# Performance work log

Measured on AMD Instinct MI355X. Metric: run time of the kernel, lower is better.

Reference implementation:

```python
import jax, jax.numpy as jnp
import numpy as np
import itertools

DIM = 384; KEY_DIM = 32; NH = 8; RES = 7; N = RES * RES
D = 4 * KEY_DIM; DH = D * NH; NHKD = KEY_DIM * NH; HID = 4 * DIM
B = 512
SCALE = KEY_DIM ** -0.5

def ste_round(x):
    return x + jax.lax.stop_gradient(jnp.round(x) - x)

def ste_floor(x):
    return x + jax.lax.stop_gradient(jnp.floor(x) - x)

def quant_act(x, bits=8):
    # dynamic per-tensor symmetric fake-quant (QuantAct)
    qmax = 2.0 ** (bits - 1) - 1
    s = jnp.maximum(jnp.max(jnp.abs(x)) / qmax, 1e-8)
    return jnp.clip(ste_round(x / s), -qmax, qmax) * s, s

def quant_w(w, bits=8):
    # per-output-channel symmetric weight fake-quant
    qmax = 2.0 ** (bits - 1) - 1
    red = tuple(range(1, w.ndim))
    s = jnp.maximum(jnp.max(jnp.abs(w), axis=red, keepdims=True) / qmax, 1e-8)
    return jnp.clip(ste_round(w / s), -qmax, qmax) * s

def conv(x, w, b, stride=1, pad=0, groups=1):
    # QuantBNConv2d with BN folded into (w, b)
    y = jax.lax.conv_general_dilated(
        x, quant_w(w), (stride, stride), [(pad, pad), (pad, pad)],
        dimension_numbers=('NCHW', 'OIHW', 'NCHW'), feature_group_count=groups)
    return y + b[None, :, None, None]

def head_mix(attn, w, b):
    # talking-heads 1x1 QuantConv2d over the head axis
    return jnp.einsum('oi,bixy->boxy', quant_w(w)[:, :, 0, 0], attn) + b[None, :, None, None]

def int_softmax(x, sf, out_bit=16):
    # I-BERT style integer softmax (2nd-order poly approx of exp) over last axis
    n = 30
    c0 = 0.35815147
    x_int = x / sf
    x_int = x_int - jnp.max(x_int, axis=-1, keepdims=True)
    x0_int = jnp.floor(-0.6931 / sf)  # ln(2) in integer domain
    x_int = jnp.maximum(x_int, n * x0_int)
    q = ste_floor(x_int / x0_int)
    r = x_int - x0_int * q
    b_int = jnp.floor((0.96963238 / c0) / sf)
    c_int = jnp.floor((1.0 / c0) / (sf * sf))
    z = (r + b_int) * r + c_int
    exp_int = jnp.clip(ste_floor(z * jnp.exp2(n - q)), 0.0, None)
    exp, exp_sf = quant_act(exp_int * (c0 * sf * sf / 2.0 ** n), 16)
    exp_int = exp / exp_sf
    factor = ste_floor(2.0 ** 32 / jnp.sum(exp_int, axis=-1, keepdims=True))
    exp_int = ste_floor(exp_int * factor / 2.0 ** (32 - out_bit))
    sf_out = 1.0 / 2.0 ** out_bit
    return exp_int * sf_out, sf_out

def _forward(x, act_sf, wq, bq, wk, bk, wv, bv, wvl, bvl, attn_biases,
             wth1, bth1, wth2, bth2, wproj, bproj,
             wfc1, bfc1, wmid, bmid, wfc2, bfc2, ls1, ls2, bias_idxs):
    Bn = x.shape[0]
    # --- token mixer (Q_Attention4D, stride=None) ---
    q, _ = quant_act(conv(x, wq, bq))
    q = q.reshape(Bn, NH, KEY_DIM, N).transpose(0, 1, 3, 2)   # (B,H,N,kd)
    k, _ = quant_act(conv(x, wk, bk))
    k = k.reshape(Bn, NH, KEY_DIM, N)                          # (B,H,kd,N)
    vf, _ = quant_act(conv(x, wv, bv))
    vl, _ = quant_act(conv(vf, wvl, bvl, pad=1, groups=DH))    # depthwise 3x3 local branch
    v = vf.reshape(Bn, NH, D, N).transpose(0, 1, 3, 2)         # (B,H,N,d)
    attn = jnp.einsum('bhnk,bhkm->bhnm', q, k) * SCALE
    attn = attn + attn_biases[:, bias_idxs]                    # (H,N,N) relative position bias
    attn, _ = quant_act(attn, 8)                               # quant_pre_th1
    attn = head_mix(attn, wth1, bth1)                          # talking_head1
    attn, a_sf = quant_act(attn, 8)                            # quant_attn
    attn, a_sf = int_softmax(attn, a_sf, 16)
    attn = head_mix(attn, wth2, bth2)                          # talking_head2
    attn, _ = quant_act(attn, 8)                               # quant_postsm
    out = jnp.einsum('bhnm,bhmd->bhnd', attn, v)
    out = out.transpose(0, 1, 3, 2).reshape(Bn, DH, RES, RES) + vl
    out, _ = quant_act(out)                                    # quant_av_res
    out = jax.nn.relu(out)                                     # proj_act
    out, _ = quant_act(out)                                    # proj_in_quant
    out = conv(out, wproj, bproj)
    out, _ = quant_act(out)                                    # proj_quant
    x1, _ = quant_act(x + ls1[None] * out)                     # residual 1 + quant_res1
    # --- Q_Mlp (mid_conv=True, ReLU) ---
    h = jax.nn.relu(conv(x1, wfc1, bfc1))
    h, _ = quant_act(h)
    h = jax.nn.relu(conv(h, wmid, bmid, pad=1, groups=HID))
    h, _ = quant_act(h)
    h = conv(h, wfc2, bfc2)
    h, _ = quant_act(h)
    out2, out_sf = quant_act(x1 + ls2[None] * h)               # residual 2 + quant_res2
    return out2, out_sf

def setup_inputs():
    key = jax.random.key(0)
    ks = jax.random.split(key, 16)
    rn = lambda k, shp: (0.02 * jax.random.normal(k, shp)).astype(jnp.float32)
    z = lambda n: jnp.zeros((n,), jnp.float32)
    # rebuild attention_bias_idxs exactly as in __init__
    pts = list(itertools.product(range(RES), range(RES)))
    offs, idxs = {}, []
    for p1 in pts:
        for p2 in pts:
            o = (abs(p1[0] - p2[0]), abs(p1[1] - p2[1]))
            if o not in offs:
                offs[o] = len(offs)
            idxs.append(offs[o])
    bias_idxs = jnp.asarray(np.array(idxs, dtype=np.int32).reshape(N, N))
    return dict(
        x=jax.random.normal(ks[0], (B, DIM, RES, RES), jnp.float32),
        act_sf=jnp.ones((1,), jnp.float32),
        wq=rn(ks[1], (NHKD, DIM, 1, 1)), bq=z(NHKD),
        wk=rn(ks[2], (NHKD, DIM, 1, 1)), bk=z(NHKD),
        wv=rn(ks[3], (DH, DIM, 1, 1)), bv=z(DH),
        wvl=rn(ks[4], (DH, 1, 3, 3)), bvl=z(DH),
        attn_biases=rn(ks[5], (NH, len(offs))),
        wth1=rn(ks[6], (NH, NH, 1, 1)), bth1=z(NH),
        wth2=rn(ks[7], (NH, NH, 1, 1)), bth2=z(NH),
        wproj=rn(ks[8], (DIM, DH, 1, 1)), bproj=z(DIM),
        wfc1=rn(ks[9], (HID, DIM, 1, 1)), bfc1=z(HID),
        wmid=rn(ks[10], (HID, 1, 3, 3)), bmid=z(HID),
        wfc2=rn(ks[11], (DIM, HID, 1, 1)), bfc2=z(DIM),
        ls1=1e-5 * jnp.ones((DIM, 1, 1), jnp.float32),
        ls2=1e-5 * jnp.ones((DIM, 1, 1), jnp.float32),
        bias_idxs=bias_idxs)

def reference(x, act_sf, wq, bq, wk, bk, wv, bv, wvl, bvl, attn_biases,
              wth1, bth1, wth2, bth2, wproj, bproj,
              wfc1, bfc1, wmid, bmid, wfc2, bfc2, ls1, ls2, bias_idxs):
    return _forward(x, act_sf, wq, bq, wk, bk, wv, bv, wvl, bvl, attn_biases,
                    wth1, bth1, wth2, bth2, wproj, bproj,
                    wfc1, bfc1, wmid, bmid, wfc2, bfc2, ls1, ls2, bias_idxs)
```

## Files before the change

kernel.cpp:

```cpp
#include <hip/hip_runtime.h>

typedef unsigned short u16;
typedef unsigned int u32;
typedef float f32x4 __attribute__((ext_vector_type(4)));
typedef short bf16x8 __attribute__((ext_vector_type(8)));
typedef short s16x4 __attribute__((ext_vector_type(4)));


__device__ __forceinline__ u16 f2bf(float f){
  u32 x = __float_as_uint(f);
  x += 0x7fffu + ((x >> 16) & 1u);
  return (u16)(x >> 16);
}
__device__ __forceinline__ float bf2f(u16 u){ return __uint_as_float(((u32)u) << 16); }
__device__ __forceinline__ float qsc(float m, float qmax){ return fmaxf(m / qmax, 1e-8f); }
__device__ __forceinline__ float fq(float x, float s){
  return fminf(fmaxf(rintf(x / s), -127.f), 127.f) * s;
}
__device__ __forceinline__ float fqi(float x, float s, float inv){
  return fminf(fmaxf(rintf(x * inv), -127.f), 127.f) * s;
}
__device__ __forceinline__ float rdmx(const float* mx, int reg){
  float m = mx[reg];
  #pragma unroll
  for (int s = 1; s < 16; ++s) m = fmaxf(m, mx[s*64 + reg]);
  return m;
}
__device__ __forceinline__ void blockMaxTo(float* mx, int reg, float v){
  __shared__ float red[8];
  #pragma unroll
  for (int o = 32; o > 0; o >>= 1) v = fmaxf(v, __shfl_xor(v, o, 64));
  const int wid = threadIdx.x >> 6;
  const int nw = (int)(blockDim.x + 63) >> 6;
  __syncthreads();
  if ((threadIdx.x & 63) == 0) red[wid] = v;
  __syncthreads();
  if (threadIdx.x == 0){
    float m = red[0];
    for (int i = 1; i < nw; ++i) m = fmaxf(m, red[i]);
    const int slot = (blockIdx.x + blockIdx.y*4) & 15;
    atomicMax((int*)&mx[slot*64 + reg], __float_as_int(m));
  }
}
__device__ __forceinline__ void blockMax2To(float* mx, int r0i, float v0, int r1i, float v1){
  __shared__ float r0[8], r1[8];
  #pragma unroll
  for (int o = 32; o > 0; o >>= 1){
    v0 = fmaxf(v0, __shfl_xor(v0, o, 64));
    v1 = fmaxf(v1, __shfl_xor(v1, o, 64));
  }
  const int wid = threadIdx.x >> 6;
  const int nw = (int)(blockDim.x + 63) >> 6;
  __syncthreads();
  if ((threadIdx.x & 63) == 0){ r0[wid] = v0; r1[wid] = v1; }
  __syncthreads();
  if (threadIdx.x == 0){
    float m0 = r0[0], m1 = r1[0];
    for (int i = 1; i < nw; ++i){ m0 = fmaxf(m0, r0[i]); m1 = fmaxf(m1, r1[i]); }
    const int slot = (blockIdx.x + blockIdx.y*4) & 15;
    atomicMax((int*)&mx[slot*64 + r0i], __float_as_int(m0));
    atomicMax((int*)&mx[slot*64 + r1i], __float_as_int(m1));
  }
}

__device__ __forceinline__ void gload16(const void* g, void* l){
  __builtin_amdgcn_global_load_lds((const __attribute__((address_space(1))) u32*)g,
                                   (__attribute__((address_space(3))) u32*)l, 16, 0, 0);
}

__global__ void zeromx(float* mx){
  for (int j = threadIdx.x; j < 1024; j += 256) mx[j] = 0.f;
}

__global__ __launch_bounds__(128) void wquant(
    const float* wq, const float* wk, const float* wv, const float* wproj,
    const float* wfc1, const float* wfc2, const float* wvl, const float* wmid,
    const float* wth1, const float* wth2,
    const float* bq, const float* bk, const float* bv,
    const float* ab, const int* idxs,
    u16* wqkv_b, u16* wproj_b, u16* wfc1_b, u16* wfc2_b,
    float* wvl_q, float* wmid_q, float* wth1_q, float* wth2_q, float* biasqkv,
    float* biasx)
{
  const int tid = threadIdx.x;
  const int bid = blockIdx.x;
  if (bid == 6416){
    for (int j = tid; j < 1536; j += 128){
      float v = (j < 256) ? bq[j] : ((j < 512) ? bk[j - 256] : bv[j - 512]);
      biasqkv[j] = v;
    }
    return;
  }
  if (bid >= 6417){
    const int h = bid - 6417;
    for (int j = tid; j < 2401; j += 128)
      biasx[h*2401 + j] = ab[h*49 + idxs[j]];
    return;
  }
  const int rows[10] = {256,256,1024,384,1536,384,1024,1536,8,8};
  int seg = 0, r = bid;
  while (r >= rows[seg]) { r -= rows[seg]; ++seg; }
  int len = 0;
  const float* src = nullptr; u16* db = nullptr; float* df = nullptr;
  switch (seg){
    case 0: len = 384;  src = wq    + r*384;  db = wqkv_b + r*384;        break;
    case 1: len = 384;  src = wk    + r*384;  db = wqkv_b + (256+r)*384;  break;
    case 2: len = 384;  src = wv    + r*384;  db = wqkv_b + (512+r)*384;  break;
    case 3: len = 1024; src = wproj + r*1024; db = wproj_b + r*1024;      break;
    case 4: len = 384;  src = wfc1  + r*384;  db = wfc1_b + r*384;        break;
    case 5: len = 1536; src = wfc2  + r*1536; db = wfc2_b + r*1536;       break;
    case 6: len = 9;    src = wvl   + r*9;    df = wvl_q + r*9;           break;
    case 7: len = 9;    src = wmid  + r*9;    df = wmid_q + r*9;          break;
    case 8: len = 8;    src = wth1  + r*8;    df = wth1_q + r*8;          break;
    default: len = 8;   src = wth2  + r*8;    df = wth2_q + r*8;          break;
  }
  float lm = 0.f;
  for (int j = tid; j < len; j += 128) lm = fmaxf(lm, fabsf(src[j]));
  __shared__ float red[128];
  red[tid] = lm; __syncthreads();
  for (int s = 64; s > 0; s >>= 1){
    if (tid < s) red[tid] = fmaxf(red[tid], red[tid + s]);
    __syncthreads();
  }
  float s = fmaxf(red[0] / 127.f, 1e-8f);
  for (int j = tid; j < len; j += 128){
    float v = fminf(fmaxf(rintf(src[j] / s), -127.f), 127.f) * s;
    if (db) db[j] = f2bf(v); else df[j] = v;
  }
}

__global__ __launch_bounds__(256) void xpose(const float* __restrict__ x, u16* __restrict__ xT){
  const int b = blockIdx.x;
  __shared__ u16 xb[18816];
  const int tid = threadIdx.x;
  for (int jj = tid; jj < 4704; jj += 256){
    const float4 v = *(const float4*)&x[(size_t)b*18816 + jj*4];
    xb[jj*4+0] = f2bf(v.x); xb[jj*4+1] = f2bf(v.y);
    xb[jj*4+2] = f2bf(v.z); xb[jj*4+3] = f2bf(v.w);
  }
  __syncthreads();
  for (int jj = tid; jj < 4704; jj += 256){
    int j = jj*4, p = j / 384, c = j - p*384;
    s16x4 o;
    #pragma unroll
    for (int u = 0; u < 4; ++u) o[u] = (short)xb[(c+u)*49 + p];
    *(s16x4*)&xT[(size_t)b*18816 + j] = o;
  }
}

__global__ __launch_bounds__(256, 3) void gemm_bt(
    const u16* __restrict__ A, const u16* __restrict__ Bt,
    const float* __restrict__ bias, u16* __restrict__ C,
    float* __restrict__ mx, int N, int K, int epi, int region, int aquant)
{
  const int nx = gridDim.x;
  const int nwg = nx * gridDim.y;
  const int orig = blockIdx.x + nx * blockIdx.y;
  const int q8 = nwg >> 3, r8 = nwg & 7;
  const int xcd = orig & 7;
  const int lid = ((xcd < r8) ? xcd*(q8+1) : r8*(q8+1) + (xcd - r8)*q8) + (orig >> 3);
  const int n0 = (lid % nx) * 128;
  const int m0 = (lid / nx) * 128;
  __shared__ __align__(16) u16 As[128*64];
  __shared__ __align__(16) u16 Bs[128*64];
  const int tid = threadIdx.x;
  const int lane = tid & 63, wid = tid >> 6;
  const int wr = wid >> 1, wc = wid & 1;
  float qa_s0 = 1.f, qa_i0 = 1.f, qa_s1 = 1.f, qa_i1 = 1.f;
  if (aquant == 1){
    qa_s0 = qsc(rdmx(mx,7), 127.f); qa_i0 = 1.f/qa_s0;
    float posq = fq(rdmx(mx,8), qa_s0);
    qa_s1 = fmaxf(posq / 127.f, 1e-8f); qa_i1 = 1.f/qa_s1;
  } else if (aquant == 2){
    qa_s0 = qsc(rdmx(mx,12), 127.f); qa_i0 = 1.f/qa_s0;
  }
  f32x4 acc[4][4] = {};
  const int nsteps = K >> 6;
  for (int s = 0; s < nsteps; ++s){
    const int k0 = s << 6;
    #pragma unroll
    for (int j = 0; j < 4; ++j){
      int boff = j*4096 + tid*16;
      int row = boff >> 7;
      int ce  = (((boff & 127) ^ ((row & 7) << 4)) >> 1);
      if (aquant == 0){
        gload16(A + (size_t)(m0 + row)*K + k0 + ce, (char*)As + boff);
      } else {
        uint4 va = *(const uint4*)(A + (size_t)(m0 + row)*K + k0 + ce);
        u16* e = (u16*)&va;
        #pragma unroll
        for (int u = 0; u < 8; ++u){
          float f = bf2f(e[u]);
          if (aquant == 1){
            f = fmaxf(fqi(f, qa_s0, qa_i0), 0.f);
            f = fqi(f, qa_s1, qa_i1);
          } else {
            f = fqi(f, qa_s0, qa_i0);
          }
          e[u] = f2bf(f);
        }
        *(uint4*)((char*)As + boff) = va;
      }
      gload16(Bt + (size_t)(n0 + row)*K + k0 + ce, (char*)Bs + boff);
    }
    __syncthreads();
    #pragma unroll
    for (int kk = 0; kk < 2; ++kk){
      bf16x8 af[4], bfr[4];
      #pragma unroll
      for (int i = 0; i < 4; ++i){
        int ar = wr*64 + i*16 + (lane & 15);
        int aidx = (ar*64 + kk*32 + (lane >> 4)*8) ^ ((ar & 7) << 3);
        af[i]  = *(const bf16x8*)&As[aidx];
        int br = wc*64 + i*16 + (lane & 15);
        int bidx = (br*64 + kk*32 + (lane >> 4)*8) ^ ((br & 7) << 3);
        bfr[i] = *(const bf16x8*)&Bs[bidx];
      }
      #pragma unroll
      for (int i = 0; i < 4; ++i){
        #pragma unroll
        for (int j = 0; j < 4; ++j){
          acc[i][j] = __builtin_amdgcn_mfma_f32_16x16x32_bf16(af[i], bfr[j], acc[i][j], 0, 0, 0);
        }
      }
    }
    __syncthreads();
  }
  float lm = 0.f;
  #pragma unroll
  for (int i = 0; i < 4; ++i){
    int rbase = m0 + wr*64 + i*16 + ((lane >> 4) << 2);
    #pragma unroll
    for (int j = 0; j < 4; ++j){
      int col = n0 + wc*64 + j*16 + (lane & 15);
      float bv = bias[col];
      #pragma unroll
      for (int q = 0; q < 4; ++q){
        float v = acc[i][j][q] + bv;
        if (epi == 2) v = fmaxf(v, 0.f);
        C[(size_t)(rbase + q)*N + col] = f2bf(v);
        lm = fmaxf(lm, (epi == 2) ? v : fabsf(v));
      }
    }
  }
  int reg = region;
  if (epi == 1) reg = (n0 < 256) ? 0 : ((n0 < 512) ? 1 : 2);
  blockMaxTo(mx, reg, lm);
}

__global__ __launch_bounds__(256) void attn_qk(
    const u16* __restrict__ qkv, const float* __restrict__ biasx,
    const float* __restrict__ wv9, const float* __restrict__ bvl,
    u16* __restrict__ S, u16* __restrict__ vlb, float* __restrict__ mx)
{
  const int h = blockIdx.x;
  __shared__ __align__(16) float xin[6272];
  __shared__ __align__(16) u16 Qb[64*40];
  __shared__ __align__(16) u16 Kb[64*40];
  const float sq = qsc(rdmx(mx,0), 127.f), sk = qsc(rdmx(mx,1), 127.f), sv = qsc(rdmx(mx,2), 127.f);
  const float iq = 1.f/sq, ik = 1.f/sk, iv = 1.f/sv;
  const int tid = threadIdx.x;
  const int lane = tid & 63, wid = tid >> 6;
  const int c = tid & 127, half = tid >> 7;
  float w9[9];
  #pragma unroll
  for (int t = 0; t < 9; ++t) w9[t] = wv9[h*1152 + c*9 + t];
  const float bb = bvl[h*128 + c];
  const float sscale = (sq * sk) * 0.17677669529663687f;
  const float* bx = biasx + h*2401;
  const int col = wid*16 + (lane & 15);
  float lm = 0.f, lmV = 0.f;
  for (int bb4 = 0; bb4 < 4; ++bb4){
    const int b = blockIdx.y*4 + bb4;
    __syncthreads();
    for (int j = tid; j < 196; j += 256){
      int n = j >> 2, d0 = (j & 3)*8;
      size_t base = (size_t)(b*49 + n)*1536;
      const bf16x8 qv = *(const bf16x8*)&qkv[base + h*32 + d0];
      const bf16x8 kv = *(const bf16x8*)&qkv[base + 256 + h*32 + d0];
      bf16x8 qo, ko;
      #pragma unroll
      for (int u = 0; u < 8; ++u){
        qo[u] = (short)f2bf(fminf(fmaxf(rintf(bf2f((u16)qv[u]) * iq), -127.f), 127.f));
        ko[u] = (short)f2bf(fminf(fmaxf(rintf(bf2f((u16)kv[u]) * ik), -127.f), 127.f));
      }
      *(bf16x8*)&Qb[n*40 + d0] = qo;
      *(bf16x8*)&Kb[n*40 + d0] = ko;
    }
    for (int j = tid; j < 784; j += 256){
      int p = j >> 4, dg = j & 15;
      const bf16x8 vv = *(const bf16x8*)&qkv[(size_t)(b*49 + p)*1536 + 512 + h*128 + dg*8];
      #pragma unroll
      for (int u = 0; u < 8; ++u)
        xin[p*128 + dg*8 + u] = fqi(bf2f((u16)vv[u]), sv, iv);
    }
    __syncthreads();
    {
      const int p0 = half*25, p1 = half ? 49 : 25;
      for (int p = p0; p < p1; ++p){
        const int py = p / 7, px = p - py*7;
        float acc = bb;
        #pragma unroll
        for (int dy = 0; dy < 3; ++dy){
          const int yy = py + dy - 1;
          if (yy < 0 || yy > 6) continue;
          #pragma unroll
          for (int dx = 0; dx < 3; ++dx){
            const int xx = px + dx - 1;
            if (xx < 0 || xx > 6) continue;
            acc += xin[(yy*7 + xx)*128 + c] * w9[dy*3 + dx];
          }
        }
        lmV = fmaxf(lmV, fabsf(acc));
        vlb[(size_t)(b*49 + p)*1024 + h*128 + c] = f2bf(acc);
      }
    }
    f32x4 acc[4] = {};
    {
      const bf16x8 bfr = *(const bf16x8*)&Kb[(wid*16 + (lane & 15))*40 + (lane >> 4)*8];
      #pragma unroll
      for (int i = 0; i < 4; ++i){
        const bf16x8 af = *(const bf16x8*)&Qb[(i*16 + (lane & 15))*40 + (lane >> 4)*8];
        acc[i] = __builtin_amdgcn_mfma_f32_16x16x32_bf16(af, bfr, acc[i], 0, 0, 0);
      }
    }
    if (col < 49){
      const size_t so = ((size_t)b*8 + h)*2401;
      #pragma unroll
      for (int i = 0; i < 4; ++i){
        #pragma unroll
        for (int q = 0; q < 4; ++q){
          const int row = i*16 + ((lane >> 4) << 2) + q;
          if (row < 49){
            float v = acc[i][q] * sscale + bx[row*49 + col];
            S[so + row*49 + col] = f2bf(v);
            lm = fmaxf(lm, fabsf(v));
          }
        }
      }
    }
  }
  blockMax2To(mx, 4, lm, 3, lmV);
}

__global__ __launch_bounds__(256) void th1k(
    const u16* S, const float* w1, const float* b1, u16* T, float* mx)
{
  const int b = blockIdx.y;
  const int j = blockIdx.x*256 + threadIdx.x;
  __shared__ float wsh[64];
  __shared__ float bsh[8];
  if (threadIdx.x < 64) wsh[threadIdx.x] = w1[threadIdx.x];
  if (threadIdx.x < 8)  bsh[threadIdx.x] = b1[threadIdx.x];
  __syncthreads();
  float lm = 0.f;
  if (j < 2401){
    const float s1 = qsc(rdmx(mx,4), 127.f);
    const float i1 = 1.f/s1;
    float a[8];
    #pragma unroll
    for (int h = 0; h < 8; ++h) a[h] = fqi(bf2f(S[((size_t)b*8 + h)*2401 + j]), s1, i1);
    float o8[8];
    #pragma unroll
    for (int o = 0; o < 8; ++o){
      float t = bsh[o];
      #pragma unroll
      for (int h = 0; h < 8; ++h) t += wsh[o*8 + h] * a[h];
      o8[o] = t;
      lm = fmaxf(lm, fabsf(t));
    }
    #pragma unroll
    for (int o = 0; o < 8; ++o) T[((size_t)b*8 + o)*2401 + j] = f2bf(o8[o]);
  }
  blockMaxTo(mx, 5, lm);
}

__global__ __launch_bounds__(256) void smth2(
    const u16* T, const float* w2, const float* b2, u16* U, float* mx)
{
  const int b = blockIdx.x;
  __shared__ u16 P[19208];
  __shared__ float wsh[64];
  __shared__ float bsh[8];
  const float sa = qsc(rdmx(mx,5), 127.f), ia = 1.f/sa;
  const int tid = threadIdx.x;
  if (tid < 64) wsh[tid] = w2[tid];
  if (tid < 8)  bsh[tid] = b2[tid];
  for (int j = tid; j < 19208; j += 256){
    float k = fminf(fmaxf(rintf(bf2f(T[(size_t)b*19208 + j]) * ia), -127.f), 127.f);
    P[j] = f2bf(k);
  }
  __syncthreads();
  const float x0 = floorf(-0.6931f / sa);
  const float ix0 = 1.f / x0;
  const float bi = floorf((0.96963238f / 0.35815147f) / sa);
  const float ci = floorf((1.0f / 0.35815147f) / (sa * sa));
  const float Kc = ((0.35815147f * sa) * sa) * (1.f/1073741824.f);
  const float maxv = (ci * 1073741824.f) * Kc;
  const float se = fmaxf(maxv / 32767.f, 1e-8f);
  const float ise = 1.f / se;
  const float clampLo = 30.f * x0;
  for (int r = tid; r < 392; r += 256){
    u16* pr = &P[r*49];
    float rmax = -1e30f;
    for (int m = 0; m < 49; ++m) rmax = fmaxf(rmax, bf2f(pr[m]));
    float rsum = 0.f;
    for (int m = 0; m < 49; ++m){
      float xi = bf2f(pr[m]) - rmax;
      xi = fmaxf(xi, clampLo);
      float qd = floorf(xi * ix0);
      float rr = xi - x0*qd;
      float z = (rr + bi)*rr + ci;
      float ei = fmaxf(floorf(z * exp2f(30.f - qd)), 0.f);
      float e2 = fminf(fmaxf(rintf((ei * Kc) * ise), -32767.f), 32767.f);
      u16 eb = f2bf(e2);
      pr[m] = eb;
      rsum += bf2f(eb);
    }
    const float factor = floorf(4294967296.f / rsum);
    for (int m = 0; m < 49; ++m){
      float p = floorf((bf2f(pr[m]) * factor) * (1.f/65536.f)) * (1.f/65536.f);
      pr[m] = f2bf(p);
    }
  }
  __syncthreads();
  float lm = 0.f;
  for (int j = tid; j < 19208; j += 256){
    int o = j / 2401, rem = j - o*2401;
    float t = bsh[o];
    #pragma unroll
    for (int h = 0; h < 8; ++h) t += wsh[o*8 + h] * bf2f(P[h*2401 + rem]);
    U[(size_t)b*19208 + j] = f2bf(t);
    lm = fmaxf(lm, fabsf(t));
  }
  blockMaxTo(mx, 6, lm);
}

__global__ __launch_bounds__(256) void attn_v(
    const u16* __restrict__ qkv, const u16* __restrict__ U,
    u16* __restrict__ av, float* __restrict__ mx)
{
  const int h = blockIdx.x, b = blockIdx.y;
  __shared__ __align__(16) u16 Pb[64*68];
  __shared__ __align__(16) u16 Vt[128*66];
  const float s3 = qsc(rdmx(mx,6), 127.f), sv = qsc(rdmx(mx,2), 127.f), svl = qsc(rdmx(mx,3), 127.f);
  const float i3 = 1.f/s3, iv = 1.f/sv, il = 1.f/svl;
  const float s3sv = s3 * sv;
  const int tid = threadIdx.x;
  const int lane = tid & 63, wid = tid >> 6;
  const int col0 = wid * 32;
  const int ca = col0 + (lane & 15), cb = ca + 16;
  u16 vlrA[16], vlrB[16];
  {
    const size_t vbase = (size_t)(b*49)*1024 + h*128;
    #pragma unroll
    for (int i = 0; i < 4; ++i){
      #pragma unroll
      for (int q = 0; q < 4; ++q){
        const int row = i*16 + ((lane >> 4) << 2) + q;
        const int rr = (row < 49) ? row : 48;
        vlrA[i*4+q] = av[vbase + (size_t)rr*1024 + ca];
        vlrB[i*4+q] = av[vbase + (size_t)rr*1024 + cb];
      }
    }
  }
  for (int j = tid; j < 64*19; j += 256){ int n = j/19, m = 49 + (j - n*19); Pb[n*68 + m] = 0; }
  for (int j = tid; j < 128*17; j += 256){ int d = j/17, m = 49 + (j - d*17); Vt[d*66 + m] = 0; }
  for (int j = tid; j < 2401; j += 256){
    int n = j / 49, m = j - n*49;
    float k = fminf(fmaxf(rintf(bf2f(U[((size_t)b*8 + h)*2401 + j]) * i3), -127.f), 127.f);
    Pb[n*68 + m] = f2bf(k);
  }
  {
    const int dp = lane * 2, mc = wid;
    const int mend = (mc == 3) ? 49 : (mc*13 + 13);
    const size_t base = (size_t)(b*49)*1536 + 512 + h*128 + dp;
    for (int m = mc*13; m < mend; ++m){
      u32 two = *(const u32*)&qkv[base + (size_t)m*1536];
      float k0 = fminf(fmaxf(rintf(bf2f((u16)(two & 0xffffu)) * iv), -127.f), 127.f);
      float k1 = fminf(fmaxf(rintf(bf2f((u16)(two >> 16)) * iv), -127.f), 127.f);
      Vt[dp*66 + m]       = f2bf(k0);
      Vt[(dp + 1)*66 + m] = f2bf(k1);
    }
  }
  __syncthreads();
  f32x4 acc[4][2] = {};
  #pragma unroll
  for (int kk = 0; kk < 2; ++kk){
    bf16x8 af[4], bfr[2];
    #pragma unroll
    for (int i = 0; i < 4; ++i)
      af[i] = *(const bf16x8*)&Pb[(i*16 + (lane & 15))*68 + kk*32 + (lane >> 4)*8];
    #pragma unroll
    for (int j = 0; j < 2; ++j)
      bfr[j] = *(const bf16x8*)&Vt[(col0 + j*16 + (lane & 15))*66 + kk*32 + (lane >> 4)*8];
    #pragma unroll
    for (int i = 0; i < 4; ++i)
      #pragma unroll
      for (int j = 0; j < 2; ++j)
        acc[i][j] = __builtin_amdgcn_mfma_f32_16x16x32_bf16(af[i], bfr[j], acc[i][j], 0, 0, 0);
  }
  float lm = 0.f, lmp = 0.f;
  #pragma unroll
  for (int i = 0; i < 4; ++i){
    #pragma unroll
    for (int q = 0; q < 4; ++q){
      const int row = i*16 + ((lane >> 4) << 2) + q;
      if (row < 49){
        const size_t base = (size_t)(b*49 + row)*1024 + h*128;
        const float vlA = fqi(bf2f(vlrA[i*4+q]), svl, il);
        const float vlB = fqi(bf2f(vlrB[i*4+q]), svl, il);
        const float vA = acc[i][0][q] * s3sv + vlA;
        const float vB = acc[i][1][q] * s3sv + vlB;
        av[base + ca] = f2bf(vA);
        av[base + cb] = f2bf(vB);
        lm = fmaxf(lm, fmaxf(fabsf(vA), fabsf(vB)));
        lmp = fmaxf(lmp, fmaxf(vA, vB));
      }
    }
  }
  blockMax2To(mx, 7, lm, 8, lmp);
}

__global__ __launch_bounds__(256) void res1max(
    const float* __restrict__ x, const u16* __restrict__ praw,
    const float* __restrict__ ls1, float* __restrict__ y1, float* __restrict__ mx)
{
  const int b = blockIdx.x;
  __shared__ float xs[18816];
  __shared__ float lss[384];
  const float sp = qsc(rdmx(mx,9), 127.f);
  const float ip = 1.f / sp;
  const int tid = threadIdx.x;
  for (int jj = tid; jj < 4704; jj += 256)
    *(float4*)&xs[jj*4] = *(const float4*)&x[(size_t)b*18816 + jj*4];
  for (int j = tid; j < 384; j += 256) lss[j] = ls1[j];
  __syncthreads();
  float lm = 0.f;
  for (int jj = tid; jj < 4704; jj += 256){
    int j = jj*4, p = j / 384, c = j - p*384;
    s16x4 pv = *(const s16x4*)&praw[(size_t)b*18816 + j];
    float4 yv;
    #pragma unroll
    for (int u = 0; u < 4; ++u){
      float y = xs[(c+u)*49 + p] + lss[c+u] * fqi(bf2f((u16)pv[u]), sp, ip);
      ((float*)&yv)[u] = y;
      lm = fmaxf(lm, fabsf(y));
    }
    *(float4*)&y1[(size_t)b*18816 + j] = yv;
  }
  blockMaxTo(mx, 10, lm);
}

__global__ void qx1(const float* __restrict__ y1, u16* __restrict__ x1b,
                    const float* __restrict__ mx){
  const float s = qsc(rdmx(mx,10), 127.f);
  const size_t n4 = (size_t)9633792/4;
  for (size_t i = (size_t)blockIdx.x*blockDim.x + threadIdx.x; i < n4; i += (size_t)gridDim.x*blockDim.x){
    float4 v = *(const float4*)(y1 + i*4);
    s16x4 ob;
    #pragma unroll
    for (int u = 0; u < 4; ++u){
      float q = fq(((const float*)&v)[u], s);
      ob[u] = (short)f2bf(q);
    }
    *(s16x4*)(x1b + i*4) = ob;
  }
}

__global__ __launch_bounds__(128) void dw_mid(
    const u16* h1, const float* wm9, const float* bmid, u16* m1, float* mx)
{
  const int cc = blockIdx.x, b = blockIdx.y;
  __shared__ float xin[49*132];
  const float sh = qsc(rdmx(mx,11), 127.f);
  const float ih = 1.f / sh;
  const int tid = threadIdx.x;
  for (int j = tid; j < 784; j += 128){
    int p = j >> 4, dg = j & 15;
    const bf16x8 vv = *(const bf16x8*)&h1[(size_t)(b*49 + p)*1536 + cc*128 + dg*8];
    #pragma unroll
    for (int u = 0; u < 8; ++u)
      xin[p*132 + dg*8 + u] = fqi(bf2f((u16)vv[u]), sh, ih);
  }
  __syncthreads();
  const int c = tid;
  float w9[9];
  #pragma unroll
  for (int i = 0; i < 9; ++i) w9[i] = wm9[(cc*128 + c)*9 + i];
  const float bb = bmid[cc*128 + c];
  float col[49];
  #pragma unroll
  for (int p = 0; p < 49; ++p) col[p] = xin[p*132 + c];
  float lm = 0.f;
  #pragma unroll
  for (int p = 0; p < 49; ++p){
    const int py = p / 7, px = p % 7;
    float acc = bb;
    #pragma unroll
    for (int dy = 0; dy < 3; ++dy){
      const int yy = py + dy - 1;
      if (yy < 0 || yy > 6) continue;
      #pragma unroll
      for (int dx = 0; dx < 3; ++dx){
        const int xx = px + dx - 1;
        if (xx < 0 || xx > 6) continue;
        acc += col[yy*7 + xx] * w9[dy*3 + dx];
      }
    }
    acc = fmaxf(acc, 0.f);
    m1[(size_t)(b*49 + p)*1536 + cc*128 + c] = f2bf(acc);
    lm = fmaxf(lm, acc);
  }
  blockMaxTo(mx, 12, lm);
}

__global__ __launch_bounds__(256) void res2max(
    const u16* __restrict__ x1b, const u16* __restrict__ f2,
    const float* __restrict__ ls2, u16* __restrict__ y2b, float* __restrict__ mx)
{
  const float s = qsc(rdmx(mx,13), 127.f);
  const float is = 1.f / s;
  float lm = 0.f;
  const size_t n8 = (size_t)9633792/8;
  for (size_t i = (size_t)blockIdx.x*blockDim.x + threadIdx.x; i < n8; i += (size_t)gridDim.x*blockDim.x){
    int c0 = (int)((i*8) % 384);
    bf16x8 xv = *(const bf16x8*)(x1b + i*8);
    bf16x8 fv = *(const bf16x8*)(f2 + i*8);
    bf16x8 yv;
    #pragma unroll
    for (int u = 0; u < 8; ++u){
      float y = bf2f((u16)xv[u]) + ls2[c0+u] * fqi(bf2f((u16)fv[u]), s, is);
      yv[u] = (short)f2bf(y);
      lm = fmaxf(lm, fabsf(y));
    }
    *(bf16x8*)(y2b + i*8) = yv;
  }
  blockMaxTo(mx, 14, lm);
}

__global__ __launch_bounds__(256) void finalout(
    const u16* __restrict__ y2b, float* __restrict__ out, const float* __restrict__ mx)
{
  const int b = blockIdx.x;
  __shared__ float os[18816];
  const float s = qsc(rdmx(mx,14), 127.f);
  const int tid = threadIdx.x;
  for (int jj = tid; jj < 4704; jj += 256){
    int j = jj*4, p = j / 384, c = j - p*384;
    s16x4 yv = *(const s16x4*)&y2b[(size_t)b*18816 + j];
    #pragma unroll
    for (int u = 0; u < 4; ++u)
      os[(c+u)*49 + p] = fq(bf2f((u16)yv[u]), s);
  }
  __syncthreads();
  for (int jj = tid; jj < 4704; jj += 256)
    *(float4*)&out[(size_t)b*18816 + jj*4] = *(const float4*)&os[jj*4];
  if (b == 0 && tid == 0) out[9633792] = s;
}

extern "C" void kernel_launch(void* const* d_in, const int* in_sizes, int n_in,
                              void* d_out, int out_size, void* d_ws, size_t ws_size,
                              hipStream_t stream)
{
  (void)in_sizes; (void)n_in; (void)out_size; (void)ws_size;
  const float* x    = (const float*)d_in[0];
  const float* wq   = (const float*)d_in[2];
  const float* bq   = (const float*)d_in[3];
  const float* wk   = (const float*)d_in[4];
  const float* bk   = (const float*)d_in[5];
  const float* wv   = (const float*)d_in[6];
  const float* bv   = (const float*)d_in[7];
  const float* wvl  = (const float*)d_in[8];
  const float* bvl  = (const float*)d_in[9];
  const float* ab   = (const float*)d_in[10];
  const float* wth1 = (const float*)d_in[11];
  const float* bth1 = (const float*)d_in[12];
  const float* wth2 = (const float*)d_in[13];
  const float* bth2 = (const float*)d_in[14];
  const float* wproj= (const float*)d_in[15];
  const float* bproj= (const float*)d_in[16];
  const float* wfc1 = (const float*)d_in[17];
  const float* bfc1 = (const float*)d_in[18];
  const float* wmid = (const float*)d_in[19];
  const float* bmid = (const float*)d_in[20];
  const float* wfc2 = (const float*)d_in[21];
  const float* bfc2 = (const float*)d_in[22];
  const float* ls1  = (const float*)d_in[23];
  const float* ls2  = (const float*)d_in[24];
  const int*   idxs = (const int*)d_in[25];
  float* out = (float*)d_out;

  char* w = (char*)d_ws;
  float* biasqkv = (float*)(w + 256);
  u16* wqkv_b    = (u16*)(w + 6400);
  u16* wproj_b   = (u16*)(w + 1186048);
  u16* wfc1_b    = (u16*)(w + 1972480);
  u16* wfc2_b    = (u16*)(w + 3152128);
  float* wvl_q   = (float*)(w + 4331776);
  float* wmid_q  = (float*)(w + 4368640);
  float* wth1_q  = (float*)(w + 4423936);
  float* wth2_q  = (float*)(w + 4424192);
  u16* xT    = (u16*)(w + 4424448);
  u16* praw  = xT;
  u16* x1b   = xT;
  u16* qkv = (u16*)(w + 23692032);
  u16* h1  = qkv;
  u16* avb = (u16*)(w + 100762368);
  u16* Sb   = (u16*)(w + 152142592);
  float* y1 = (float*)(w + 152142592);
  u16* f2raw = (u16*)(w + 152142592);
  u16* y2b   = (u16*)(w + 152142592 + 19267584);
  float* biasx = (float*)(w + 190677760);
  float* mx = (float*)(w + 190754816);

  zeromx<<<1, 256, 0, stream>>>(mx);
  wquant<<<6425, 128, 0, stream>>>(wq, wk, wv, wproj, wfc1, wfc2, wvl, wmid, wth1, wth2,
                                   bq, bk, bv, ab, idxs,
                                   wqkv_b, wproj_b, wfc1_b, wfc2_b,
                                   wvl_q, wmid_q, wth1_q, wth2_q, biasqkv, biasx);
  xpose<<<512, 256, 0, stream>>>(x, xT);
  gemm_bt<<<dim3(12, 196), 256, 0, stream>>>(xT, wqkv_b, biasqkv, qkv, mx, 1536, 384, 1, 0, 0);
  attn_qk<<<dim3(8, 128), 256, 0, stream>>>(qkv, biasx, wvl_q, bvl, Sb, avb, mx);
  th1k<<<dim3(10, 512), 256, 0, stream>>>(Sb, wth1_q, bth1, Sb, mx);
  smth2<<<512, 256, 0, stream>>>(Sb, wth2_q, bth2, Sb, mx);
  attn_v<<<dim3(8, 512), 256, 0, stream>>>(qkv, Sb, avb, mx);
  gemm_bt<<<dim3(3, 196), 256, 0, stream>>>(avb, wproj_b, bproj, praw, mx, 384, 1024, 0, 9, 1);
  res1max<<<512, 256, 0, stream>>>(x, praw, ls1, y1, mx);
  qx1<<<2048, 256, 0, stream>>>(y1, x1b, mx);
  gemm_bt<<<dim3(12, 196), 256, 0, stream>>>(x1b, wfc1_b, bfc1, h1, mx, 1536, 384, 2, 11, 0);
  dw_mid<<<dim3(12, 512), 128, 0, stream>>>(h1, wmid_q, bmid, h1, mx);
  gemm_bt<<<dim3(3, 196), 256, 0, stream>>>(h1, wfc2_b, bfc2, f2raw, mx, 384, 1536, 0, 13, 2);
  res2max<<<2048, 256, 0, stream>>>(x1b, f2raw, ls2, y2b, mx);
  finalout<<<512, 256, 0, stream>>>(y2b, out, mx);
}
```

Before: 526.8 us.

## Add double-buffered direct-to-LDS GEMM with XCD-aware tile remap for QKV and FC1

Adds a new gemm_p kernel with double-buffered LDS tiles of K=32, filled through async global-to-LDS loads. Each step waits on vmcnt, so the next tile's load overlaps the current MFMA step. It also remaps workgroup IDs so neighbouring tiles land on the same XCD, uses a new swizzle pattern, and sets launch bounds for 3 blocks per CU. The two wide-N GEMMs (QKV and FC1) switch to it. The risk is that the smaller K step adds more barriers per step, and the hand-written waitcnt may be fragile.

```diff
diff --git a/kernel.cpp b/kernel.cpp
--- a/kernel.cpp
+++ b/kernel.cpp
@@ -225,6 +225,96 @@
       }
     }
     __syncthreads();
+  }
+  float lm = 0.f;
+  #pragma unroll
+  for (int i = 0; i < 4; ++i){
+    int rbase = m0 + wr*64 + i*16 + ((lane >> 4) << 2);
+    #pragma unroll
+    for (int j = 0; j < 4; ++j){
+      int col = n0 + wc*64 + j*16 + (lane & 15);
+      float bv = bias[col];
+      #pragma unroll
+      for (int q = 0; q < 4; ++q){
+        float v = acc[i][j][q] + bv;
+        if (epi == 2) v = fmaxf(v, 0.f);
+        C[(size_t)(rbase + q)*N + col] = f2bf(v);
+        lm = fmaxf(lm, (epi == 2) ? v : fabsf(v));
+      }
+    }
+  }
+  int reg = region;
+  if (epi == 1) reg = (n0 < 256) ? 0 : ((n0 < 512) ? 1 : 2);
+  blockMaxTo(mx, reg, lm);
+}
+
+__global__ __launch_bounds__(256, 3) void gemm_p(
+    const u16* __restrict__ A, const u16* __restrict__ Bt,
+    const float* __restrict__ bias, u16* __restrict__ C,
+    float* __restrict__ mx, int N, int K, int epi, int region)
+{
+  const int nx = gridDim.x;
+  const int nwg = nx * gridDim.y;
+  const int orig = blockIdx.x + nx * blockIdx.y;
+  const int q8 = nwg >> 3, r8 = nwg & 7;
+  const int xcd = orig & 7;
+  const int lid = ((xcd < r8) ? xcd*(q8+1) : r8*(q8+1) + (xcd - r8)*q8) + (orig >> 3);
+  const int n0 = (lid % nx) * 128;
+  const int m0 = (lid / nx) * 128;
+  __shared__ __align__(16) u16 As[2][128*32];
+  __shared__ __align__(16) u16 Bs[2][128*32];
+  const int tid = threadIdx.x;
+  const int lane = tid & 63, wid = tid >> 6;
+  const int wr = wid >> 1, wc = wid & 1;
+  f32x4 acc[4][4] = {};
+  const int nsteps = K >> 5;
+  int srow[2], scol[2], sboff[2];
+  #pragma unroll
+  for (int r = 0; r < 2; ++r){
+    int boff = r*4096 + tid*16;
+    int row = boff >> 6;
+    int slot = (boff >> 4) & 3;
+    sboff[r] = boff;
+    srow[r] = row;
+    scol[r] = (slot ^ ((row >> 1) & 3)) << 3;
+  }
+  #pragma unroll
+  for (int r = 0; r < 2; ++r){
+    gload16(A  + (size_t)(m0 + srow[r])*K + scol[r], (char*)As[0] + sboff[r]);
+    gload16(Bt + (size_t)(n0 + srow[r])*K + scol[r], (char*)Bs[0] + sboff[r]);
+  }
+  for (int s = 0; s < nsteps; ++s){
+    const int cur = s & 1;
+    if (s + 1 < nsteps){
+      const int k1 = (s + 1) << 5;
+      #pragma unroll
+      for (int r = 0; r < 2; ++r){
+        gload16(A  + (size_t)(m0 + srow[r])*K + k1 + scol[r], (char*)As[cur ^ 1] + sboff[r]);
+        gload16(Bt + (size_t)(n0 + srow[r])*K + k1 + scol[r], (char*)Bs[cur ^ 1] + sboff[r]);
+      }
+      asm volatile("s_waitcnt vmcnt(4)" ::: "memory");
+    } else {
+      asm volatile("s_waitcnt vmcnt(0)" ::: "memory");
+    }
+    asm volatile("s_barrier" ::: "memory");
+    bf16x8 af[4], bfr[4];
+    #pragma unroll
+    for (int i = 0; i < 4; ++i){
+      int ar = wr*64 + i*16 + (lane & 15);
+      int ab2 = ar*64 + ((((lane >> 4) ^ ((ar >> 1) & 3))) << 4);
+      af[i]  = *(const bf16x8*)((const char*)As[cur] + ab2);
+      int br = wc*64 + i*16 + (lane & 15);
+      int bb2 = br*64 + ((((lane >> 4) ^ ((br >> 1) & 3))) << 4);
+      bfr[i] = *(const bf16x8*)((const char*)Bs[cur] + bb2);
+    }
+    #pragma unroll
+    for (int i = 0; i < 4; ++i){
+      #pragma unroll
+      for (int j = 0; j < 4; ++j){
+        acc[i][j] = __builtin_amdgcn_mfma_f32_16x16x32_bf16(af[i], bfr[j], acc[i][j], 0, 0, 0);
+      }
+    }
+    asm volatile("s_barrier" ::: "memory");
   }
   float lm = 0.f;
   #pragma unroll
@@ -720,7 +810,7 @@
                                    wqkv_b, wproj_b, wfc1_b, wfc2_b,
                                    wvl_q, wmid_q, wth1_q, wth2_q, biasqkv, biasx);
   xpose<<<512, 256, 0, stream>>>(x, xT);
-  gemm_bt<<<dim3(12, 196), 256, 0, stream>>>(xT, wqkv_b, biasqkv, qkv, mx, 1536, 384, 1, 0, 0);
+  gemm_p<<<dim3(12, 196), 256, 0, stream>>>(xT, wqkv_b, biasqkv, qkv, mx, 1536, 384, 1, 0);
   attn_qk<<<dim3(8, 128), 256, 0, stream>>>(qkv, biasx, wvl_q, bvl, Sb, avb, mx);
   th1k<<<dim3(10, 512), 256, 0, stream>>>(Sb, wth1_q, bth1, Sb, mx);
   smth2<<<512, 256, 0, stream>>>(Sb, wth2_q, bth2, Sb, mx);
@@ -728,7 +818,7 @@
   gemm_bt<<<dim3(3, 196), 256, 0, stream>>>(avb, wproj_b, bproj, praw, mx, 384, 1024, 0, 9, 1);
   res1max<<<512, 256, 0, stream>>>(x, praw, ls1, y1, mx);
   qx1<<<2048, 256, 0, stream>>>(y1, x1b, mx);
-  gemm_bt<<<dim3(12, 196), 256, 0, stream>>>(x1b, wfc1_b, bfc1, h1, mx, 1536, 384, 2, 11, 0);
+  gemm_p<<<dim3(12, 196), 256, 0, stream>>>(x1b, wfc1_b, bfc1, h1, mx, 1536, 384, 2, 11);
   dw_mid<<<dim3(12, 512), 128, 0, stream>>>(h1, wmid_q, bmid, h1, mx);
   gemm_bt<<<dim3(3, 196), 256, 0, stream>>>(h1, wfc2_b, bfc2, f2raw, mx, 384, 1536, 0, 13, 2);
   res2max<<<2048, 256, 0, stream>>>(x1b, f2raw, ls2, y2b, mx);
```

Result: slower. 541.8 us (+2.8%).
